# Kernel tuning notes

Measured on AMD Instinct MI355X. Metric: run time of the kernel, lower is better.

## Reference

```python
import jax, jax.numpy as jnp
import numpy as np

N = 100000          # nodes
E = 1600000         # edges
NODE_DIM = 128
HID = 64
NUM_LAYERS = 3
G = 256             # graphs in batch
BN_EPS = 1e-5


def setup_inputs() -> dict:
    key = jax.random.key(0)
    ks = jax.random.split(key, 20)
    x = jax.random.normal(ks[0], (N, NODE_DIM), dtype=jnp.float32)
    edge_index = jax.random.randint(ks[1], (2, E), 0, N, dtype=jnp.int64)
    batch = jnp.sort(jax.random.randint(ks[2], (N,), 0, G, dtype=jnp.int64))
    s_in = 1.0 / np.sqrt(NODE_DIM)
    s_h = 1.0 / np.sqrt(HID)
    W_in = jax.random.uniform(ks[3], (NODE_DIM, HID), jnp.float32, -s_in, s_in)
    b_in = jax.random.uniform(ks[4], (HID,), jnp.float32, -s_in, s_in)
    conv_W = jax.random.uniform(ks[5], (NUM_LAYERS, HID, HID), jnp.float32, -s_h, s_h)
    conv_b = jax.random.uniform(ks[6], (NUM_LAYERS, HID), jnp.float32, -s_h, s_h)
    bn_gamma = jnp.ones((NUM_LAYERS, HID), jnp.float32)
    bn_beta = jnp.zeros((NUM_LAYERS, HID), jnp.float32)
    bn_mean = 0.1 * jax.random.normal(ks[7], (NUM_LAYERS, HID), jnp.float32)
    bn_var = jnp.ones((NUM_LAYERS, HID), jnp.float32) + 0.1 * jax.random.uniform(ks[8], (NUM_LAYERS, HID))
    W1 = jax.random.uniform(ks[9], (HID, HID), jnp.float32, -s_h, s_h)
    b1 = jax.random.uniform(ks[10], (HID,), jnp.float32, -s_h, s_h)
    W2 = jax.random.uniform(ks[11], (HID, HID // 2), jnp.float32, -s_h, s_h)
    b2 = jax.random.uniform(ks[12], (HID // 2,), jnp.float32, -s_h, s_h)
    s_h2 = 1.0 / np.sqrt(HID // 2)
    W3 = jax.random.uniform(ks[13], (HID // 2, 1), jnp.float32, -s_h2, s_h2)
    b3 = jax.random.uniform(ks[14], (1,), jnp.float32, -s_h2, s_h2)
    return dict(x=x, edge_index=edge_index, batch=batch, W_in=W_in, b_in=b_in,
                conv_W=conv_W, conv_b=conv_b, bn_gamma=bn_gamma, bn_beta=bn_beta,
                bn_mean=bn_mean, bn_var=bn_var, W1=W1, b1=b1, W2=W2, b2=b2, W3=W3, b3=b3)


def reference(x, edge_index, batch, W_in, b_in, conv_W, conv_b,
              bn_gamma, bn_beta, bn_mean, bn_var, W1, b1, W2, b2, W3, b3):
    n = x.shape[0]
    loop = jnp.arange(n, dtype=edge_index.dtype)
    src = jnp.concatenate([edge_index[0], loop])   # edges + self loops
    dst = jnp.concatenate([edge_index[1], loop])
    deg = jax.ops.segment_sum(jnp.ones_like(src, dtype=x.dtype), dst, num_segments=n)
    dinv = jax.lax.rsqrt(jnp.maximum(deg, 1.0))
    norm = (dinv[src] * dinv[dst])[:, None]        # [E+N, 1] sym-normalized edge weight

    h = x @ W_in + b_in                            # input projection [N, HID]
    for l in range(NUM_LAYERS):
        hw = h @ conv_W[l]                         # GCNConv: transform then aggregate
        agg = jax.ops.segment_sum(hw[src] * norm, dst, num_segments=n) + conv_b[l]
        # BatchNorm (eval: running stats) + ReLU; dropout is identity in eval
        hnorm = (agg - bn_mean[l]) * jax.lax.rsqrt(bn_var[l] + BN_EPS)
        h = jax.nn.relu(hnorm * bn_gamma[l] + bn_beta[l])

    # global mean pool over graphs
    sums = jax.ops.segment_sum(h, batch, num_segments=G)
    cnts = jax.ops.segment_sum(jnp.ones((n,), h.dtype), batch, num_segments=G)
    g = sums / jnp.maximum(cnts, 1.0)[:, None]     # [G, HID]

    g = jax.nn.relu(g @ W1 + b1)
    g = jax.nn.relu(g @ W2 + b2)
    out = g @ W3 + b3                              # [G, 1]
    return out.squeeze(-1)
```

## Files before the change

### kernel.cpp

```cpp
#include <hip/hip_runtime.h>
#include <hip/hip_bf16.h>

#define NN 100000
#define EE 1600000
#define NODE_DIM 128
#define HID 64
#define NGRAPH 256
#define BN_EPS 1e-5f

#define NB 196
#define BW 512
#define CH 4096
#define NCHUNK 391
#define MHIST (NB * NCHUNK)
#define MAXB 12288

typedef __attribute__((ext_vector_type(8))) short short8;
typedef __attribute__((ext_vector_type(4))) float f32x4;

static __device__ __forceinline__ unsigned short f2bf(float f) {
    unsigned u = __float_as_uint(f);
    unsigned r = (u + 0x7fffu + ((u >> 16) & 1u)) >> 16;
    return (unsigned short)r;
}
static __device__ __forceinline__ float bf2f(unsigned short u) {
    return __uint_as_float(((unsigned)u) << 16);
}

#define I_OFF   0
#define I_DEG   100032
#define I_HIST  200064
#define I_HS    276864
#define I_BS    353664
#define I_BO    353792
#define I_PAIR  353920
#define I_SRCS  3553920
#define I_DINV  5153920
#define I_WC    5253952
#define I_WFA   5262208
#define I_WF1   5266304
#define I_WF2   5268352
#define I_BUFA  5270400
#define I_BUFB  8470400
#define I_SUMS  11670400
#define I_SCSH  11686784

__global__ __launch_bounds__(256) void hist_k(const int* __restrict__ dst,
                                              int* __restrict__ hist) {
    __shared__ int h[NB];
    for (int i = threadIdx.x; i < NB; i += 256) h[i] = 0;
    __syncthreads();
    int base = blockIdx.x * CH + threadIdx.x;
    #pragma unroll
    for (int j = 0; j < 16; ++j) {
        int e = base + j * 256;
        if (e < EE) {
            int d = __builtin_nontemporal_load(dst + e);
            atomicAdd(&h[d >> 9], 1);
        }
    }
    __syncthreads();
    for (int i = threadIdx.x; i < NB; i += 256)
        hist[i * NCHUNK + blockIdx.x] = h[i];
}

__global__ void scan1_k(const int* __restrict__ in, int* __restrict__ part,
                        int* __restrict__ bsums, int n) {
    __shared__ int wsum[4];
    __shared__ int woff[4];
    int t = threadIdx.x;
    int base = blockIdx.x * 1024 + t * 4;
    int v0 = 0, v1 = 0, v2 = 0, v3 = 0;
    if (base + 3 < n) {
        v0 = in[base]; v1 = in[base + 1]; v2 = in[base + 2]; v3 = in[base + 3];
    } else {
        if (base     < n) v0 = in[base];
        if (base + 1 < n) v1 = in[base + 1];
        if (base + 2 < n) v2 = in[base + 2];
    }
    int s = v0 + v1 + v2 + v3;
    int lane = t & 63, wid = t >> 6;
    int x = s;
    #pragma unroll
    for (int d = 1; d < 64; d <<= 1) {
        int y = __shfl_up(x, d, 64);
        if (lane >= d) x += y;
    }
    if (lane == 63) wsum[wid] = x;
    __syncthreads();
    if (t == 0) {
        int r = 0;
        for (int w = 0; w < 4; ++w) { woff[w] = r; r += wsum[w]; }
        bsums[blockIdx.x] = r;
    }
    __syncthreads();
    int ex = woff[wid] + (x - s);
    if (base     < n) part[base]     = ex;
    if (base + 1 < n) part[base + 1] = ex + v0;
    if (base + 2 < n) part[base + 2] = ex + v0 + v1;
    if (base + 3 < n) part[base + 3] = ex + v0 + v1 + v2;
}

__global__ void scan2_k(const int* __restrict__ bsums, int* __restrict__ boffs, int nb) {
    __shared__ int wsum[2];
    __shared__ int woff2[2];
    int t = threadIdx.x;
    int v = (t < nb) ? bsums[t] : 0;
    int lane = t & 63, wid = t >> 6;
    int x = v;
    #pragma unroll
    for (int d = 1; d < 64; d <<= 1) {
        int y = __shfl_up(x, d, 64);
        if (lane >= d) x += y;
    }
    if (lane == 63) wsum[wid] = x;
    __syncthreads();
    if (t == 0) { woff2[0] = 0; woff2[1] = wsum[0]; }
    __syncthreads();
    int ex = woff2[wid] + (x - v);
    if (t < nb) boffs[t] = ex;
}

__global__ void scan3g_k(int* __restrict__ arr, const int* __restrict__ boffs, int n) {
    int i = blockIdx.x * 256 + threadIdx.x;
    if (i < n) arr[i] += boffs[i >> 10];
}

__global__ __launch_bounds__(256) void sortB_k(const int* __restrict__ srcA,
                                               const int* __restrict__ dstA,
                                               const int* __restrict__ hs,
                                               int2* __restrict__ pair) {
    __shared__ int lcur[NB];
    for (int i = threadIdx.x; i < NB; i += 256)
        lcur[i] = hs[i * NCHUNK + blockIdx.x];
    __syncthreads();
    int base = blockIdx.x * CH + threadIdx.x;
    #pragma unroll
    for (int j = 0; j < 16; ++j) {
        int e = base + j * 256;
        if (e < EE) {
            int d = __builtin_nontemporal_load(dstA + e);
            int s = __builtin_nontemporal_load(srcA + e);
            int pos = atomicAdd(&lcur[d >> 9], 1);
            pair[pos] = make_int2(d, s);
        }
    }
}

__global__ __launch_bounds__(256) void fineC_k(const int2* __restrict__ pair,
                                               const int* __restrict__ hs,
                                               int* __restrict__ deg,
                                               int* __restrict__ off,
                                               int* __restrict__ csrc) {
    __shared__ int cnt[BW];
    __shared__ int loff[BW];
    __shared__ int wsum[4];
    __shared__ int woff[4];
    __shared__ int ssrc[MAXB];
    int b = blockIdx.x;
    int t = threadIdx.x;
    int base = hs[b * NCHUNK];
    int end  = (b == NB - 1) ? EE : hs[(b + 1) * NCHUNK];
    int m = end - base;

    for (int i = t; i < BW; i += 256) cnt[i] = 0;
    __syncthreads();
    for (int i = t; i < m; i += 256) {
        int2 p = pair[base + i];
        atomicAdd(&cnt[p.x & (BW - 1)], 1);
    }
    __syncthreads();

    int c0 = cnt[2 * t], c1 = cnt[2 * t + 1];
    int s = c0 + c1;
    int lane = t & 63, wid = t >> 6;
    int x = s;
    #pragma unroll
    for (int d = 1; d < 64; d <<= 1) {
        int y = __shfl_up(x, d, 64);
        if (lane >= d) x += y;
    }
    if (lane == 63) wsum[wid] = x;
    __syncthreads();
    if (t == 0) {
        int r = 0;
        for (int w = 0; w < 4; ++w) { woff[w] = r; r += wsum[w]; }
    }
    __syncthreads();
    int ex = woff[wid] + (x - s);
    loff[2 * t] = ex;
    loff[2 * t + 1] = ex + c0;
    __syncthreads();

    int node0 = b << 9;
    for (int i = t; i < BW; i += 256) {
        int node = node0 + i;
        if (node < NN) { deg[node] = cnt[i]; off[node] = base + loff[i]; }
        else if (node == NN) { off[NN] = EE; }
    }
    __syncthreads();

    for (int i = t; i < BW; i += 256) cnt[i] = loff[i];
    __syncthreads();
    for (int i = t; i < m; i += 256) {
        int2 p = pair[base + i];
        int pos = atomicAdd(&cnt[p.x & (BW - 1)], 1);
        if (pos < MAXB) ssrc[pos] = p.y;
        else            csrc[base + pos] = p.y;
    }
    __syncthreads();
    int mm = m < MAXB ? m : MAXB;
    for (int i = t; i < mm; i += 256) csrc[base + i] = ssrc[i];
}

__global__ void dinv_k(const int* __restrict__ cnt, float* __restrict__ dinv, int n) {
    int i = blockIdx.x * 256 + threadIdx.x;
    if (i < n) dinv[i] = rsqrtf((float)(cnt[i] + 1));
}

__global__ void bnprep_k(const float* __restrict__ convb, const float* __restrict__ gamma,
                         const float* __restrict__ beta, const float* __restrict__ mean,
                         const float* __restrict__ var, float* __restrict__ scsh) {
    int t = blockIdx.x * 64 + threadIdx.x;
    int l = t >> 6, c = t & 63;
    float sc = gamma[l * 64 + c] * rsqrtf(var[l * 64 + c] + BN_EPS);
    float sh = (convb[l * 64 + c] - mean[l * 64 + c]) * sc + beta[l * 64 + c];
    scsh[l * 128 + c] = sc;
    scsh[l * 128 + 64 + c] = sh;
}

__global__ void wc_k(const float* __restrict__ Win, const float* __restrict__ bin,
                     const float* __restrict__ cw0, float* __restrict__ Wc) {
    int idx = blockIdx.x * 256 + threadIdx.x;
    if (idx < NODE_DIM * HID) {
        int k = idx >> 6, c = idx & 63;
        float a = 0.f;
        #pragma unroll 8
        for (int j = 0; j < HID; ++j) a += Win[k * HID + j] * cw0[j * HID + c];
        Wc[idx] = a;
    } else if (idx < NODE_DIM * HID + HID) {
        int c = idx - NODE_DIM * HID;
        float a = 0.f;
        #pragma unroll 8
        for (int j = 0; j < HID; ++j) a += bin[j] * cw0[j * HID + c];
        Wc[idx] = a;
    }
}

__global__ __launch_bounds__(256) void wfrag_k(const float* __restrict__ Wc,
                                               const float* __restrict__ convW,
                                               short* __restrict__ WfA,
                                               short* __restrict__ Wf1,
                                               short* __restrict__ Wf2) {
    int id = blockIdx.x * 256 + threadIdx.x;
    const float* W; short* out; int u;
    if (id < 1024)      { W = Wc;           out = WfA; u = id; }
    else if (id < 1536) { W = convW + 4096; out = Wf1; u = id - 1024; }
    else                { W = convW + 8192; out = Wf2; u = id - 1536; }
    int l = u & 63, t = (u >> 6) & 3, s = u >> 8;
    int k0 = s * 32 + ((l >> 4) & 3) * 8;
    int col = t * 16 + (l & 15);
    short8 v;
    #pragma unroll
    for (int j = 0; j < 8; ++j) v[j] = (short)f2bf(W[(k0 + j) * 64 + col]);
    *(short8*)(out + u * 8) = v;
}

template <int K, bool BIAS, bool A_BF16>
__global__ __launch_bounds__(256, 4) void gemm_k(const void* __restrict__ inv,
                                                 const short8* __restrict__ Wf,
                                                 const float* __restrict__ bias,
                                                 __hip_bfloat16* __restrict__ out) {
    constexpr int NS = K / 32;
    int l = threadIdx.x & 63;
    int w = threadIdx.x >> 6;
    int rows0 = blockIdx.x * 64 + w * 16;
    int arow = rows0 + (l & 15);
    bool rok = arow < NN;
    int kgrp = (l >> 4) & 3;

    short8 wf[NS][4];
    #pragma unroll
    for (int s = 0; s < NS; ++s)
        #pragma unroll
        for (int t = 0; t < 4; ++t)
            wf[s][t] = Wf[(s * 4 + t) * 64 + l];

    f32x4 acc[4];
    #pragma unroll
    for (int t = 0; t < 4; ++t) acc[t] = (f32x4){0.f, 0.f, 0.f, 0.f};

    #pragma unroll
    for (int s = 0; s < NS; ++s) {
        short8 af = {0, 0, 0, 0, 0, 0, 0, 0};
        if (A_BF16) {
            if (rok)
                af = *(const short8*)((const short*)inv + (long)arow * K + s * 32 + kgrp * 8);
        } else {
            if (rok) {
                const float* ap = (const float*)inv + (long)arow * K + s * 32 + kgrp * 8;
                float4 a0 = *(const float4*)ap;
                float4 a1 = *(const float4*)(ap + 4);
                af[0] = (short)f2bf(a0.x); af[1] = (short)f2bf(a0.y);
                af[2] = (short)f2bf(a0.z); af[3] = (short)f2bf(a0.w);
                af[4] = (short)f2bf(a1.x); af[5] = (short)f2bf(a1.y);
                af[6] = (short)f2bf(a1.z); af[7] = (short)f2bf(a1.w);
            }
        }
        #pragma unroll
        for (int t = 0; t < 4; ++t)
            acc[t] = __builtin_amdgcn_mfma_f32_16x16x32_bf16(af, wf[s][t], acc[t], 0, 0, 0);
    }

    int orow0 = rows0 + kgrp * 4;
    #pragma unroll
    for (int t = 0; t < 4; ++t) {
        int col = t * 16 + (l & 15);
        float b = BIAS ? bias[col] : 0.f;
        #pragma unroll
        for (int r = 0; r < 4; ++r) {
            int row = orow0 + r;
            if (row < NN)
                out[(long)row * HID + col] = __float2bfloat16(acc[t][r] + b);
        }
    }
}

__global__ __launch_bounds__(256) void aggregate_k(const unsigned short* __restrict__ hw,
                                                   const int* __restrict__ off,
                                                   const int* __restrict__ src,
                                                   const float* __restrict__ dinv,
                                                   const float* __restrict__ scsh,
                                                   unsigned short* __restrict__ out) {
    int lane = threadIdx.x & 63;
    int q = lane >> 4;
    int c4 = (lane & 15) * 4;
    int i = __builtin_amdgcn_readfirstlane((int)blockIdx.x * 4 + (threadIdx.x >> 6));
    float di = dinv[i];
    int e0 = off[i], e1 = off[i + 1];

    float a0 = 0.f, a1 = 0.f, a2 = 0.f, a3 = 0.f;
    float b0 = 0.f, b1 = 0.f, b2 = 0.f, b3 = 0.f;

    if (q == 0) {
        ushort4 h = *(const ushort4*)(hw + (long)i * HID + c4);
        float wgt = di * di;
        a0 += bf2f(h.x) * wgt; a1 += bf2f(h.y) * wgt;
        a2 += bf2f(h.z) * wgt; a3 += bf2f(h.w) * wgt;
    }

    int nit = (e1 - e0 + 3) >> 2;
    int it = 0;
    for (; it + 2 <= nit; it += 2) {
        int ea = e0 + it * 4 + q;
        int eb = ea + 4;
        bool oka = ea < e1, okb = eb < e1;
        int sa = src[oka ? ea : e0];
        int sb = src[okb ? eb : e0];
        float wa = oka ? dinv[sa] * di : 0.f;
        float wb = okb ? dinv[sb] * di : 0.f;
        ushort4 ha = *(const ushort4*)(hw + (long)sa * HID + c4);
        ushort4 hb = *(const ushort4*)(hw + (long)sb * HID + c4);
        a0 += bf2f(ha.x) * wa; a1 += bf2f(ha.y) * wa;
        a2 += bf2f(ha.z) * wa; a3 += bf2f(ha.w) * wa;
        b0 += bf2f(hb.x) * wb; b1 += bf2f(hb.y) * wb;
        b2 += bf2f(hb.z) * wb; b3 += bf2f(hb.w) * wb;
    }
    if (it < nit) {
        int ea = e0 + it * 4 + q;
        bool oka = ea < e1;
        int sa = src[oka ? ea : e0];
        float wa = oka ? dinv[sa] * di : 0.f;
        ushort4 ha = *(const ushort4*)(hw + (long)sa * HID + c4);
        a0 += bf2f(ha.x) * wa; a1 += bf2f(ha.y) * wa;
        a2 += bf2f(ha.z) * wa; a3 += bf2f(ha.w) * wa;
    }
    a0 += b0; a1 += b1; a2 += b2; a3 += b3;

    a0 += __shfl_xor(a0, 16, 64); a1 += __shfl_xor(a1, 16, 64);
    a2 += __shfl_xor(a2, 16, 64); a3 += __shfl_xor(a3, 16, 64);
    a0 += __shfl_xor(a0, 32, 64); a1 += __shfl_xor(a1, 32, 64);
    a2 += __shfl_xor(a2, 32, 64); a3 += __shfl_xor(a3, 32, 64);

    if (q == 0) {
        float4 sc = *(const float4*)(scsh + c4);
        float4 sh = *(const float4*)(scsh + 64 + c4);
        ushort4 o;
        o.x = f2bf(fmaxf(a0 * sc.x + sh.x, 0.f));
        o.y = f2bf(fmaxf(a1 * sc.y + sh.y, 0.f));
        o.z = f2bf(fmaxf(a2 * sc.z + sh.z, 0.f));
        o.w = f2bf(fmaxf(a3 * sc.w + sh.w, 0.f));
        *(ushort4*)(out + (long)i * HID + c4) = o;
    }
}

__global__ __launch_bounds__(256) void pool1_k(const __hip_bfloat16* __restrict__ h,
                                               const int* __restrict__ batch,
                                               float* __restrict__ sums) {
    int lane = threadIdx.x & 63;
    int wid = threadIdx.x >> 6;
    int chunk = blockIdx.x * 4 + wid;
    int i0 = chunk * 64;
    if (i0 >= NN) return;
    int i1 = i0 + 64;
    if (i1 > NN) i1 = NN;
    int g = batch[i0];
    float acc = 0.f;
    for (int i = i0; i < i1; ++i) {
        int bi = batch[i];
        if (bi != g) {
            atomicAdd(&sums[g * HID + lane], acc);
            acc = 0.f;
            g = bi;
        }
        acc += __bfloat162float(h[(long)i * HID + lane]);
    }
    atomicAdd(&sums[g * HID + lane], acc);
}

__device__ __forceinline__ int lower_bound_i(const int* __restrict__ a, int n, int key) {
    int lo = 0, hi = n;
    while (lo < hi) {
        int m = (lo + hi) >> 1;
        if (a[m] < key) lo = m + 1; else hi = m;
    }
    return lo;
}

__global__ __launch_bounds__(64) void mlp_k(const float* __restrict__ sums,
                                            const int* __restrict__ batch,
                                            const float* __restrict__ W1, const float* __restrict__ b1,
                                            const float* __restrict__ W2, const float* __restrict__ b2,
                                            const float* __restrict__ W3, const float* __restrict__ b3,
                                            float* __restrict__ out) {
    int g = blockIdx.x;
    int lane = threadIdx.x;
    int start = lower_bound_i(batch, NN, g);
    int end = lower_bound_i(batch, NN, g + 1);
    float cnt = (float)(end - start);
    float gv = sums[g * HID + lane] / fmaxf(cnt, 1.0f);

    __shared__ float gs[HID];
    __shared__ float h1s[HID];
    gs[lane] = gv;
    __syncthreads();

    float a1 = b1[lane];
    #pragma unroll 8
    for (int k = 0; k < HID; ++k) a1 += gs[k] * W1[k * HID + lane];
    a1 = fmaxf(a1, 0.f);
    h1s[lane] = a1;
    __syncthreads();

    float a2 = 0.f;
    if (lane < 32) {
        a2 = b2[lane];
        #pragma unroll 8
        for (int k = 0; k < HID; ++k) a2 += h1s[k] * W2[k * 32 + lane];
        a2 = fmaxf(a2, 0.f);
    }
    float p = (lane < 32) ? a2 * W3[lane] : 0.f;
    #pragma unroll
    for (int d = 32; d >= 1; d >>= 1) p += __shfl_down(p, d, 64);
    if (lane == 0) out[g] = p + b3[0];
}

extern "C" void kernel_launch(void* const* d_in, const int* in_sizes, int n_in,
                              void* d_out, int out_size, void* d_ws, size_t ws_size,
                              hipStream_t stream) {
    (void)in_sizes; (void)n_in; (void)out_size; (void)ws_size;

    const float* x      = (const float*)d_in[0];
    const int*   eidx   = (const int*)d_in[1];
    const int*   batch  = (const int*)d_in[2];
    const float* W_in   = (const float*)d_in[3];
    const float* b_in   = (const float*)d_in[4];
    const float* conv_W = (const float*)d_in[5];
    const float* conv_b = (const float*)d_in[6];
    const float* gamma  = (const float*)d_in[7];
    const float* beta   = (const float*)d_in[8];
    const float* mean   = (const float*)d_in[9];
    const float* var    = (const float*)d_in[10];
    const float* W1     = (const float*)d_in[11];
    const float* b1     = (const float*)d_in[12];
    const float* W2     = (const float*)d_in[13];
    const float* b2     = (const float*)d_in[14];
    const float* W3     = (const float*)d_in[15];
    const float* b3     = (const float*)d_in[16];
    float* outp = (float*)d_out;

    int*   wsi = (int*)d_ws;
    float* wsf = (float*)d_ws;

    int*   off    = wsi + I_OFF;
    int*   deg    = wsi + I_DEG;
    int*   hist   = wsi + I_HIST;
    int*   hs     = wsi + I_HS;
    int*   bsums  = wsi + I_BS;
    int*   boffs  = wsi + I_BO;
    int2*  pair   = (int2*)(wsi + I_PAIR);
    int*   csrc   = wsi + I_SRCS;
    float* dinv   = wsf + I_DINV;
    float* Wc     = wsf + I_WC;
    short* WfA    = (short*)(wsi + I_WFA);
    short* Wf1    = (short*)(wsi + I_WF1);
    short* Wf2    = (short*)(wsi + I_WF2);
    __hip_bfloat16* bufA = (__hip_bfloat16*)(wsf + I_BUFA);
    __hip_bfloat16* bufB = (__hip_bfloat16*)(wsf + I_BUFB);
    float* sums   = wsf + I_SUMS;
    float* scsh   = wsf + I_SCSH;

    const int* esrc = eidx;
    const int* edst = eidx + EE;

    hipMemsetAsync(sums, 0, NGRAPH * HID * sizeof(float), stream);

    hist_k<<<NCHUNK, 256, 0, stream>>>(edst, hist);
    int nb1 = (MHIST + 1023) / 1024;
    scan1_k<<<nb1, 256, 0, stream>>>(hist, hs, bsums, MHIST);
    scan2_k<<<1, 128, 0, stream>>>(bsums, boffs, nb1);
    scan3g_k<<<(MHIST + 255) / 256, 256, 0, stream>>>(hs, boffs, MHIST);
    wc_k<<<(NODE_DIM * HID + HID + 255) / 256, 256, 0, stream>>>(W_in, b_in, conv_W, Wc);
    wfrag_k<<<8, 256, 0, stream>>>(Wc, conv_W, WfA, Wf1, Wf2);
    bnprep_k<<<3, 64, 0, stream>>>(conv_b, gamma, beta, mean, var, scsh);
    sortB_k<<<NCHUNK, 256, 0, stream>>>(esrc, edst, hs, pair);
    fineC_k<<<NB, 256, 0, stream>>>(pair, hs, deg, off, csrc);
    dinv_k<<<(NN + 255) / 256, 256, 0, stream>>>(deg, dinv, NN);

    int ngemm = (NN + 63) / 64;
    gemm_k<NODE_DIM, true, false><<<ngemm, 256, 0, stream>>>(x, (const short8*)WfA,
                                                             Wc + NODE_DIM * HID, bufA);
    aggregate_k<<<NN / 4, 256, 0, stream>>>((const unsigned short*)bufA, off, csrc, dinv,
                                            scsh + 0 * 128, (unsigned short*)bufB);
    gemm_k<HID, false, true><<<ngemm, 256, 0, stream>>>(bufB, (const short8*)Wf1, nullptr, bufA);
    aggregate_k<<<NN / 4, 256, 0, stream>>>((const unsigned short*)bufA, off, csrc, dinv,
                                            scsh + 1 * 128, (unsigned short*)bufB);
    gemm_k<HID, false, true><<<ngemm, 256, 0, stream>>>(bufB, (const short8*)Wf2, nullptr, bufA);
    aggregate_k<<<NN / 4, 256, 0, stream>>>((const unsigned short*)bufA, off, csrc, dinv,
                                            scsh + 2 * 128, (unsigned short*)bufB);

    pool1_k<<<(NN / 64 + 3) / 4, 256, 0, stream>>>(bufB, batch, sums);
    mlp_k<<<NGRAPH, 64, 0, stream>>>(sums, batch, W1, b1, W2, b2, W3, b3, outp);
}
```

Measured before the change: 438.4 us.

## Precompute per-edge source weights and restructure aggregation to one column per lane

Adds a kernel that gathers dinv[src] into a per-edge weight array once, so the three aggregation passes read weights contiguously instead of doing a dependent random gather. The aggregation kernel is rewritten so each lane owns one feature column and the whole wavefront walks edges in batches of eight, loading eight source rows at once. This drops the cross-quarter shuffle reduction and raises memory-level parallelism. The trade-offs are one extra 1.6M-element pass and memory buffer, and 2-byte per-lane gathers instead of 8-byte vector loads.

```diff
diff --git a/kernel.cpp b/kernel.cpp
--- a/kernel.cpp
+++ b/kernel.cpp
@@ -44,6 +44,7 @@
 #define I_BUFB  8470400
 #define I_SUMS  11670400
 #define I_SCSH  11686784
+#define I_WS    11687168
 
 __global__ __launch_bounds__(256) void hist_k(const int* __restrict__ dst,
                                               int* __restrict__ hist) {
@@ -216,6 +217,12 @@
 __global__ void dinv_k(const int* __restrict__ cnt, float* __restrict__ dinv, int n) {
     int i = blockIdx.x * 256 + threadIdx.x;
     if (i < n) dinv[i] = rsqrtf((float)(cnt[i] + 1));
+}
+
+__global__ void wsrc_k(const int* __restrict__ csrc, const float* __restrict__ dinv,
+                       float* __restrict__ ws) {
+    int e = blockIdx.x * 256 + threadIdx.x;
+    if (e < EE) ws[e] = dinv[csrc[e]];
 }
 
 __global__ void bnprep_k(const float* __restrict__ convb, const float* __restrict__ gamma,
@@ -329,69 +336,40 @@
 __global__ __launch_bounds__(256) void aggregate_k(const unsigned short* __restrict__ hw,
                                                    const int* __restrict__ off,
                                                    const int* __restrict__ src,
+                                                   const float* __restrict__ ws,
                                                    const float* __restrict__ dinv,
                                                    const float* __restrict__ scsh,
                                                    unsigned short* __restrict__ out) {
     int lane = threadIdx.x & 63;
-    int q = lane >> 4;
-    int c4 = (lane & 15) * 4;
     int i = __builtin_amdgcn_readfirstlane((int)blockIdx.x * 4 + (threadIdx.x >> 6));
     float di = dinv[i];
     int e0 = off[i], e1 = off[i + 1];
 
-    float a0 = 0.f, a1 = 0.f, a2 = 0.f, a3 = 0.f;
-    float b0 = 0.f, b1 = 0.f, b2 = 0.f, b3 = 0.f;
-
-    if (q == 0) {
-        ushort4 h = *(const ushort4*)(hw + (long)i * HID + c4);
-        float wgt = di * di;
-        a0 += bf2f(h.x) * wgt; a1 += bf2f(h.y) * wgt;
-        a2 += bf2f(h.z) * wgt; a3 += bf2f(h.w) * wgt;
-    }
-
-    int nit = (e1 - e0 + 3) >> 2;
-    int it = 0;
-    for (; it + 2 <= nit; it += 2) {
-        int ea = e0 + it * 4 + q;
-        int eb = ea + 4;
-        bool oka = ea < e1, okb = eb < e1;
-        int sa = src[oka ? ea : e0];
-        int sb = src[okb ? eb : e0];
-        float wa = oka ? dinv[sa] * di : 0.f;
-        float wb = okb ? dinv[sb] * di : 0.f;
-        ushort4 ha = *(const ushort4*)(hw + (long)sa * HID + c4);
-        ushort4 hb = *(const ushort4*)(hw + (long)sb * HID + c4);
-        a0 += bf2f(ha.x) * wa; a1 += bf2f(ha.y) * wa;
-        a2 += bf2f(ha.z) * wa; a3 += bf2f(ha.w) * wa;
-        b0 += bf2f(hb.x) * wb; b1 += bf2f(hb.y) * wb;
-        b2 += bf2f(hb.z) * wb; b3 += bf2f(hb.w) * wb;
-    }
-    if (it < nit) {
-        int ea = e0 + it * 4 + q;
-        bool oka = ea < e1;
-        int sa = src[oka ? ea : e0];
-        float wa = oka ? dinv[sa] * di : 0.f;
-        ushort4 ha = *(const ushort4*)(hw + (long)sa * HID + c4);
-        a0 += bf2f(ha.x) * wa; a1 += bf2f(ha.y) * wa;
-        a2 += bf2f(ha.z) * wa; a3 += bf2f(ha.w) * wa;
-    }
-    a0 += b0; a1 += b1; a2 += b2; a3 += b3;
-
-    a0 += __shfl_xor(a0, 16, 64); a1 += __shfl_xor(a1, 16, 64);
-    a2 += __shfl_xor(a2, 16, 64); a3 += __shfl_xor(a3, 16, 64);
-    a0 += __shfl_xor(a0, 32, 64); a1 += __shfl_xor(a1, 32, 64);
-    a2 += __shfl_xor(a2, 32, 64); a3 += __shfl_xor(a3, 32, 64);
-
-    if (q == 0) {
-        float4 sc = *(const float4*)(scsh + c4);
-        float4 sh = *(const float4*)(scsh + 64 + c4);
-        ushort4 o;
-        o.x = f2bf(fmaxf(a0 * sc.x + sh.x, 0.f));
-        o.y = f2bf(fmaxf(a1 * sc.y + sh.y, 0.f));
-        o.z = f2bf(fmaxf(a2 * sc.z + sh.z, 0.f));
-        o.w = f2bf(fmaxf(a3 * sc.w + sh.w, 0.f));
-        *(ushort4*)(out + (long)i * HID + c4) = o;
-    }
+    float acc = bf2f(hw[(long)i * HID + lane]) * di * di;
+
+    int nit = (e1 - e0 + 7) >> 3;
+    for (int it = 0; it < nit; ++it) {
+        int eb = e0 + it * 8;
+        int sx[8]; float wx[8];
+        #pragma unroll
+        for (int j = 0; j < 8; ++j) {
+            int ee = eb + j;
+            bool ok = ee < e1;
+            sx[j] = src[ok ? ee : e0];
+            wx[j] = ok ? ws[ee] * di : 0.f;
+        }
+        float h[8];
+        #pragma unroll
+        for (int j = 0; j < 8; ++j)
+            h[j] = bf2f(hw[(long)sx[j] * HID + lane]);
+        #pragma unroll
+        for (int j = 0; j < 8; ++j)
+            acc += h[j] * wx[j];
+    }
+
+    float sc = scsh[lane];
+    float sh = scsh[64 + lane];
+    out[(long)i * HID + lane] = f2bf(fmaxf(acc * sc + sh, 0.f));
 }
 
 __global__ __launch_bounds__(256) void pool1_k(const __hip_bfloat16* __restrict__ h,
@@ -509,6 +487,7 @@
     __hip_bfloat16* bufB = (__hip_bfloat16*)(wsf + I_BUFB);
     float* sums   = wsf + I_SUMS;
     float* scsh   = wsf + I_SCSH;
+    float* ws     = wsf + I_WS;
 
     const int* esrc = eidx;
     const int* edst = eidx + EE;
@@ -526,17 +505,18 @@
     sortB_k<<<NCHUNK, 256, 0, stream>>>(esrc, edst, hs, pair);
     fineC_k<<<NB, 256, 0, stream>>>(pair, hs, deg, off, csrc);
     dinv_k<<<(NN + 255) / 256, 256, 0, stream>>>(deg, dinv, NN);
+    wsrc_k<<<(EE + 255) / 256, 256, 0, stream>>>(csrc, dinv, ws);
 
     int ngemm = (NN + 63) / 64;
     gemm_k<NODE_DIM, true, false><<<ngemm, 256, 0, stream>>>(x, (const short8*)WfA,
                                                              Wc + NODE_DIM * HID, bufA);
-    aggregate_k<<<NN / 4, 256, 0, stream>>>((const unsigned short*)bufA, off, csrc, dinv,
+    aggregate_k<<<NN / 4, 256, 0, stream>>>((const unsigned short*)bufA, off, csrc, ws, dinv,
                                             scsh + 0 * 128, (unsigned short*)bufB);
     gemm_k<HID, false, true><<<ngemm, 256, 0, stream>>>(bufB, (const short8*)Wf1, nullptr, bufA);
-    aggregate_k<<<NN / 4, 256, 0, stream>>>((const unsigned short*)bufA, off, csrc, dinv,
+    aggregate_k<<<NN / 4, 256, 0, stream>>>((const unsigned short*)bufA, off, csrc, ws, dinv,
                                             scsh + 1 * 128, (unsigned short*)bufB);
     gemm_k<HID, false, true><<<ngemm, 256, 0, stream>>>(bufB, (const short8*)Wf2, nullptr, bufA);
-    aggregate_k<<<NN / 4, 256, 0, stream>>>((const unsigned short*)bufA, off, csrc, dinv,
+    aggregate_k<<<NN / 4, 256, 0, stream>>>((const unsigned short*)bufA, off, csrc, ws, dinv,
                                             scsh + 2 * 128, (unsigned short*)bufB);
 
     pool1_k<<<(NN / 64 + 3) / 4, 256, 0, stream>>>(bufB, batch, sums);
```

Result: slower. 455.7 us (+3.9%).
